# Performance work log

Measured on AMD Instinct MI355X. Metric: run time of the kernel, lower is better.

Reference implementation:

```python
import jax, jax.numpy as jnp
import numpy as np
from jax import lax

LATENT = 128
CODEBOOK = 1024

def _conv(x, w, b):
    # NCHW conv, kernel OIHW, stride 1, padding 1 (same)
    y = lax.conv_general_dilated(x, w, (1, 1), ((1, 1), (1, 1)),
                                 dimension_numbers=('NCHW', 'OIHW', 'NCHW'))
    return y + b[None, :, None, None]

def _conv_transpose(x, w, b):
    # ConvTranspose2d(k=3, s=1, p=1) == conv with flipped kernel, in/out swapped, pad 1
    w_eff = jnp.flip(w, (2, 3)).transpose(1, 0, 2, 3)  # [Cin,Cout,3,3] -> [Cout,Cin,3,3]
    return _conv(x, w_eff, b)

def _maxpool2(x):
    return lax.reduce_window(x, -jnp.inf, lax.max, (1, 1, 2, 2), (1, 1, 2, 2), 'VALID')

def _upsample2(x):
    # F.interpolate(scale_factor=2), default nearest
    return jnp.repeat(jnp.repeat(x, 2, axis=2), 2, axis=3)

def setup_inputs() -> dict:
    key = jax.random.key(0)
    ks = jax.random.split(key, 20)
    f = jnp.float32
    inp = {
        'x': jax.random.uniform(ks[0], (8192, 1, 24, 24), dtype=f),
        'conv1_w': jax.random.normal(ks[1], (32, 1, 3, 3), f) * 0.1,
        'conv1_b': jnp.zeros((32,), f),
        'conv2_w': jax.random.normal(ks[2], (64, 32, 3, 3), f) * 0.05,
        'conv2_b': jnp.zeros((64,), f),
        'conv3_w': jax.random.normal(ks[3], (128, 64, 3, 3), f) * 0.04,
        'conv3_b': jnp.zeros((128,), f),
        'enc_fc_w': jax.random.normal(ks[4], (LATENT, 3 * 3 * 128), f) * 0.03,
        'enc_fc_b': jnp.zeros((LATENT,), f),
        'codebook': jax.random.normal(ks[5], (CODEBOOK, LATENT), f),
        'dec_fc_w': jax.random.normal(ks[6], (3 * 3 * 128, LATENT), f) * 0.09,
        'dec_fc_b': jnp.zeros((3 * 3 * 128,), f),
        'dct1_w': jax.random.normal(ks[7], (128, 64, 3, 3), f) * 0.03,  # [Cin,Cout,kh,kw]
        'dct1_b': jnp.zeros((64,), f),
        'dct2_w': jax.random.normal(ks[8], (64, 32, 3, 3), f) * 0.04,
        'dct2_b': jnp.zeros((32,), f),
        'dct3_w': jax.random.normal(ks[9], (32, 1, 3, 3), f) * 0.06,
        'dct3_b': jnp.zeros((1,), f),
    }
    return inp

def reference(x, conv1_w, conv1_b, conv2_w, conv2_b, conv3_w, conv3_b,
              enc_fc_w, enc_fc_b, codebook, dec_fc_w, dec_fc_b,
              dct1_w, dct1_b, dct2_w, dct2_b, dct3_w, dct3_b):
    # ---- Encoder ----
    h = _maxpool2(jax.nn.relu(_conv(x, conv1_w, conv1_b)))     # [B,32,12,12]
    h = _maxpool2(jax.nn.relu(_conv(h, conv2_w, conv2_b)))     # [B,64,6,6]
    h = _maxpool2(jax.nn.relu(_conv(h, conv3_w, conv3_b)))     # [B,128,3,3]
    z = h.reshape(-1, 3 * 3 * 128) @ enc_fc_w.T + enc_fc_b     # [B,128]
    # ---- Quantize (L2 nearest-codeword; matmul-trick distances, same argmin) ----
    d2 = (jnp.sum(z * z, axis=1, keepdims=True)
          - 2.0 * z @ codebook.T
          + jnp.sum(codebook * codebook, axis=1)[None, :])     # [B,K]
    idx = jnp.argmin(d2, axis=1)                               # [B]
    z_q = codebook[idx]                                        # [B,128]
    # ---- Decoder ----
    d = z_q @ dec_fc_w.T + dec_fc_b                            # [B,1152]
    d = d.reshape(-1, 128, 3, 3)
    d = _upsample2(jax.nn.relu(_conv_transpose(d, dct1_w, dct1_b)))  # [B,64,6,6]
    d = _upsample2(jax.nn.relu(_conv_transpose(d, dct2_w, dct2_b)))  # [B,32,12,12]
    d = _upsample2(jax.nn.relu(_conv_transpose(d, dct3_w, dct3_b)))  # [B,1,24,24]
    return d
```

## Files before the change

### kernel.cpp

```cpp
#include <hip/hip_runtime.h>

typedef __attribute__((ext_vector_type(8))) short short8;
typedef __attribute__((ext_vector_type(4))) float f32x4;
typedef unsigned short ushort_t;
typedef unsigned int uint_t;

#define OFF_W1R   0
#define OFF_W2R   288
#define OFF_W3R   (288+18432)
#define OFF_EWT   (18720+73728)
#define OFF_CT    (92448+147456)
#define OFF_CC    (239904+131072)
#define OFF_DWT   (370976+1024)
#define OFF_D1R   (372000+147456)
#define OFF_D2R   (519456+73728)
#define OFF_D3R   (593184+18432)
#define WS_WEIGHTS (611616+288)
#define OFF_W2BF  WS_WEIGHTS
#define OFF_W3BF  (OFF_W2BF+18432)
#define OFF_H     (OFF_W3BF+73728)
#define OFF_TABLE OFF_H
#define OFF_IDSN  (OFF_H+8192*1152)

__device__ __forceinline__ ushort_t f2bf(float v) {
  uint_t u = __float_as_uint(v);
  return (ushort_t)((u + 0x7FFFu + ((u >> 16) & 1u)) >> 16);
}
__device__ __forceinline__ float bf2f(ushort_t b) {
  return __uint_as_float(((uint_t)b) << 16);
}

__global__ void vq_prep(const float* __restrict__ conv1_w, const float* __restrict__ conv2_w,
                        const float* __restrict__ conv3_w, const float* __restrict__ enc_fc_w,
                        const float* __restrict__ codebook, const float* __restrict__ dec_fc_w,
                        const float* __restrict__ dct1_w, const float* __restrict__ dct2_w,
                        const float* __restrict__ dct3_w, float* __restrict__ ws) {
  int i = blockIdx.x * blockDim.x + threadIdx.x;
  if (i >= WS_WEIGHTS) return;
  if (i < OFF_W2R) {
    int tap = i >> 5, co = i & 31;
    ws[i] = conv1_w[co*9 + tap];
  } else if (i < OFF_W3R) {
    int l = i - OFF_W2R;
    int co = l & 63, r = l >> 6, tap = r % 9, ci = r / 9;
    ws[i] = conv2_w[(co*32 + ci)*9 + tap];
  } else if (i < OFF_EWT) {
    int l = i - OFF_W3R;
    int co = l & 127, r = l >> 7, tap = r % 9, ci = r / 9;
    ws[i] = conv3_w[(co*64 + ci)*9 + tap];
  } else if (i < OFF_CC) {
    return;
  } else if (i < OFF_DWT) {
    int k = i - OFF_CC;
    float s = 0.f;
    for (int j = 0; j < 128; ++j) { float v = codebook[k*128+j]; s += v*v; }
    ws[i] = s;
  } else if (i < OFF_D1R) {
    int l = i - OFF_DWT;
    int j = l % 1152, k = l / 1152;
    ws[i] = dec_fc_w[j*128 + k];
  } else if (i < OFF_D2R) {
    int l = i - OFF_D1R;
    int co = l & 63, r = l >> 6, tap = r % 9, ci = r / 9;
    ws[i] = dct1_w[(ci*64 + co)*9 + (8 - tap)];
  } else if (i < OFF_D3R) {
    int l = i - OFF_D2R;
    int co = l & 31, r = l >> 5, tap = r % 9, ci = r / 9;
    ws[i] = dct2_w[(ci*32 + co)*9 + (8 - tap)];
  } else {
    int l = i - OFF_D3R;
    int tap = l % 9, ci = l / 9;
    ws[i] = dct3_w[ci*9 + (8 - tap)];
  }
}

__global__ void vq_prep2(const float* __restrict__ conv2_w, const float* __restrict__ conv3_w,
                         float* __restrict__ ws) {
  int i = blockIdx.x * blockDim.x + threadIdx.x;
  ushort_t* W2 = (ushort_t*)(ws + OFF_W2BF);
  ushort_t* W3 = (ushort_t*)(ws + OFF_W3BF);
  if (i < 18432) {
    int tap = i >> 11, r = i & 2047, co = r >> 5, ch = r & 31;
    float v = conv2_w[(co*32 + ch)*9 + tap];
    ushort_t hb = f2bf(v);
    W2[i] = hb; W2[18432 + i] = f2bf(v - bf2f(hb));
  } else if (i < 92160) {
    int j = i - 18432;
    int tap = j >> 13, r = j & 8191, co = r >> 6, ch = r & 63;
    float v = conv3_w[(co*64 + ch)*9 + tap];
    ushort_t hb = f2bf(v);
    W3[j] = hb; W3[73728 + j] = f2bf(v - bf2f(hb));
  }
}

__global__ __launch_bounds__(256, 3) void vq_enc(
    const float* __restrict__ x,
    const float* __restrict__ b1, const float* __restrict__ b2, const float* __restrict__ b3,
    const float* __restrict__ ws, float* __restrict__ hout)
{
  __shared__ ushort_t R0h[7840], R0l[7840];
  __shared__ ushort_t C3h[4608], C3l[4608];
  __shared__ float XT[624];
  const int t = threadIdx.x;
  const int b = blockIdx.x;

  for (int i = t; i < 3920; i += 256) { ((uint_t*)R0h)[i] = 0u; ((uint_t*)R0l)[i] = 0u; }
  for (int i = t; i < 2304; i += 256) { ((uint_t*)C3h)[i] = 0u; ((uint_t*)C3l)[i] = 0u; }
  const float* xb = x + (size_t)b * 576;
  for (int i = t; i < 624; i += 256) {
    int row = i / 26, col = i - row * 26;
    XT[i] = (col >= 1 && col <= 24) ? xb[row*24 + col - 1] : 0.f;
  }
  __syncthreads();

  {
    int co = t & 31, g = t >> 5, gy = g >> 1, gx = g & 1;
    float w[9];
    #pragma unroll
    for (int k = 0; k < 9; ++k) w[k] = ws[OFF_W1R + k*32 + co];
    float bias = b1[co];
    #pragma unroll
    for (int pr = 0; pr < 3; ++pr) {
      int Y = gy*6 + pr*2;
      float a0[12], a1[12];
      #pragma unroll
      for (int i = 0; i < 12; ++i) { a0[i] = 0.f; a1[i] = 0.f; }
      #pragma unroll
      for (int wy = 0; wy < 4; ++wy) {
        int ry = Y - 1 + wy;
        if (ry < 0 || ry > 23) continue;
        const float2* rp = (const float2*)&XT[ry*26 + gx*12];
        float r[14];
        #pragma unroll
        for (int k = 0; k < 7; ++k) { float2 p = rp[k]; r[2*k] = p.x; r[2*k+1] = p.y; }
        if (wy < 3) {
          #pragma unroll
          for (int xx = 0; xx < 12; ++xx)
            #pragma unroll
            for (int dx = 0; dx < 3; ++dx) a0[xx] += r[xx+dx] * w[wy*3+dx];
        }
        if (wy >= 1) {
          #pragma unroll
          for (int xx = 0; xx < 12; ++xx)
            #pragma unroll
            for (int dx = 0; dx < 3; ++dx) a1[xx] += r[xx+dx] * w[(wy-1)*3+dx];
        }
      }
      #pragma unroll
      for (int pc = 0; pc < 6; ++pc) {
        float m = fmaxf(fmaxf(a0[2*pc], a0[2*pc+1]), fmaxf(a1[2*pc], a1[2*pc+1]));
        float v = m + bias; v = v > 0.f ? v : 0.f;
        int row = gy*3 + pr, colp = gx*6 + pc;
        int addr = ((row+1)*14 + (colp+1))*40 + co;
        ushort_t hb = f2bf(v);
        R0h[addr] = hb;
        R0l[addr] = f2bf(v - bf2f(hb));
      }
    }
  }
  __syncthreads();

  const int lane = t & 63, quad = lane >> 4, col = lane & 15;
  const int wv = t >> 6;

  {
    const int h = wv & 1, p = wv >> 1;
    const ushort_t* W2 = (const ushort_t*)(ws + OFF_W2BF);
    int baseA[5];
    #pragma unroll
    for (int mi = 0; mi < 5; ++mi) {
      int m = (h*5 + mi)*16 + col; if (m > 143) m = 143;
      int cell = m >> 2, sub = m & 3;
      int opy = cell / 6, opx = cell - opy*6;
      int y = 2*opy + (sub >> 1), xx = 2*opx + (sub & 1);
      baseA[mi] = (y*14 + xx)*40 + quad*8;
    }
    f32x4 acc[5][2];
    #pragma unroll
    for (int mi = 0; mi < 5; ++mi) { acc[mi][0] = (f32x4)0.f; acc[mi][1] = (f32x4)0.f; }
    const int co0 = p*32 + col, co1 = co0 + 16;
    #pragma unroll
    for (int t9 = 0; t9 < 9; ++t9) {
      const int TAPOFF = ((t9/3)*14 + (t9%3))*40;
      int bidx = t9*2048 + quad*8;
      short8 Bh0 = *(const short8*)(W2 + bidx + co0*32);
      short8 Bh1 = *(const short8*)(W2 + bidx + co1*32);
      short8 Bl0 = *(const short8*)(W2 + 18432 + bidx + co0*32);
      short8 Bl1 = *(const short8*)(W2 + 18432 + bidx + co1*32);
      #pragma unroll
      for (int mi = 0; mi < 5; ++mi) {
        int a = baseA[mi] + TAPOFF;
        short8 Ah = *(const short8*)(R0h + a);
        short8 Al = *(const short8*)(R0l + a);
        acc[mi][0] = __builtin_amdgcn_mfma_f32_16x16x32_bf16(Al, Bh0, acc[mi][0], 0, 0, 0);
        acc[mi][0] = __builtin_amdgcn_mfma_f32_16x16x32_bf16(Ah, Bl0, acc[mi][0], 0, 0, 0);
        acc[mi][0] = __builtin_amdgcn_mfma_f32_16x16x32_bf16(Ah, Bh0, acc[mi][0], 0, 0, 0);
        acc[mi][1] = __builtin_amdgcn_mfma_f32_16x16x32_bf16(Al, Bh1, acc[mi][1], 0, 0, 0);
        acc[mi][1] = __builtin_amdgcn_mfma_f32_16x16x32_bf16(Ah, Bl1, acc[mi][1], 0, 0, 0);
        acc[mi][1] = __builtin_amdgcn_mfma_f32_16x16x32_bf16(Ah, Bh1, acc[mi][1], 0, 0, 0);
      }
    }
    #pragma unroll
    for (int mi = 0; mi < 5; ++mi) {
      int cell = (h*5 + mi)*4 + quad;
      if (cell < 36) {
        int opy = cell / 6, opx = cell - opy*6;
        int wa = ((opy+1)*8 + (opx+1))*72;
        #pragma unroll
        for (int j = 0; j < 2; ++j) {
          int ch = j ? co1 : co0;
          f32x4 a = acc[mi][j];
          float v = fmaxf(fmaxf(a.x, a.y), fmaxf(a.z, a.w)) + b2[ch];
          v = v > 0.f ? v : 0.f;
          ushort_t hb = f2bf(v);
          C3h[wa + ch] = hb;
          C3l[wa + ch] = f2bf(v - bf2f(hb));
        }
      }
    }
  }
  __syncthreads();

  {
    const ushort_t* W3 = (const ushort_t*)(ws + OFF_W3BF);
    int baseA[3];
    #pragma unroll
    for (int mt = 0; mt < 3; ++mt) {
      int m = mt*16 + col; if (m > 35) m = 35;
      int cell = m >> 2, sub = m & 3;
      int opy = cell / 3, opx = cell - opy*3;
      int y = 2*opy + (sub >> 1), xx = 2*opx + (sub & 1);
      baseA[mt] = (y*8 + xx)*72 + quad*8;
    }
    f32x4 acc[3][2];
    #pragma unroll
    for (int mt = 0; mt < 3; ++mt) { acc[mt][0] = (f32x4)0.f; acc[mt][1] = (f32x4)0.f; }
    const int co0 = wv*16 + col, co1 = co0 + 64;
    #pragma unroll
    for (int ks = 0; ks < 18; ++ks) {
      const int t9 = ks >> 1, ch0 = (ks & 1)*32;
      const int TAPOFF = ((t9/3)*8 + (t9%3))*72;
      int bidx = t9*8192 + ch0 + quad*8;
      short8 Bh0 = *(const short8*)(W3 + bidx + co0*64);
      short8 Bh1 = *(const short8*)(W3 + bidx + co1*64);
      short8 Bl0 = *(const short8*)(W3 + 73728 + bidx + co0*64);
      short8 Bl1 = *(const short8*)(W3 + 73728 + bidx + co1*64);
      #pragma unroll
      for (int mt = 0; mt < 3; ++mt) {
        int a = baseA[mt] + TAPOFF + ch0;
        short8 Ah = *(const short8*)(C3h + a);
        short8 Al = *(const short8*)(C3l + a);
        acc[mt][0] = __builtin_amdgcn_mfma_f32_16x16x32_bf16(Al, Bh0, acc[mt][0], 0, 0, 0);
        acc[mt][0] = __builtin_amdgcn_mfma_f32_16x16x32_bf16(Ah, Bl0, acc[mt][0], 0, 0, 0);
        acc[mt][0] = __builtin_amdgcn_mfma_f32_16x16x32_bf16(Ah, Bh0, acc[mt][0], 0, 0, 0);
        acc[mt][1] = __builtin_amdgcn_mfma_f32_16x16x32_bf16(Al, Bh1, acc[mt][1], 0, 0, 0);
        acc[mt][1] = __builtin_amdgcn_mfma_f32_16x16x32_bf16(Ah, Bl1, acc[mt][1], 0, 0, 0);
        acc[mt][1] = __builtin_amdgcn_mfma_f32_16x16x32_bf16(Ah, Bh1, acc[mt][1], 0, 0, 0);
      }
    }
    float* hb_ = hout + (size_t)b * 1152;
    #pragma unroll
    for (int mt = 0; mt < 3; ++mt) {
      int cell = mt*4 + quad;
      if (cell < 9) {
        #pragma unroll
        for (int j = 0; j < 2; ++j) {
          int ch = j ? co1 : co0;
          f32x4 a = acc[mt][j];
          float v = fmaxf(fmaxf(a.x, a.y), fmaxf(a.z, a.w)) + b3[ch];
          v = v > 0.f ? v : 0.f;
          hb_[ch*9 + cell] = v;
        }
      }
    }
  }
}

__global__ __launch_bounds__(256, 2) void vq_fc_argmin(
    const float* __restrict__ efw, const float* __restrict__ efb,
    const float* __restrict__ cb, const float* __restrict__ ws,
    const float* __restrict__ h, int* __restrict__ ids)
{
  __shared__ float HT[18432];
  __shared__ float WVs[64];
  __shared__ int   WIs[64];
  const int t = threadIdx.x;
  const int sb = blockIdx.x * 16;

  const float4* src = (const float4*)(h + (size_t)sb * 1152);
  for (int i = t; i < 4608; i += 256) ((float4*)HT)[i] = src[i];
  __syncthreads();

  const int j = t & 127, g = t >> 7;
  float acc[8];
  #pragma unroll
  for (int u = 0; u < 8; ++u) acc[u] = 0.f;
  const float* wj = efw + (size_t)j * 1152;
  for (int k4 = 0; k4 < 1152; k4 += 4) {
    float4 wvv = *(const float4*)(wj + k4);
    const float* hp = &HT[g*9216 + k4];
    #pragma unroll
    for (int u = 0; u < 8; ++u) {
      float4 hv = *(const float4*)(hp + u*1152);
      acc[u] += wvv.x*hv.x + wvv.y*hv.y + wvv.z*hv.z + wvv.w*hv.w;
    }
  }
  float bias = efb[j];
  __syncthreads();
  #pragma unroll
  for (int u = 0; u < 8; ++u) HT[(g*8 + u)*128 + j] = acc[u] + bias;
  __syncthreads();

  float bestv[16]; int besti[16];
  #pragma unroll
  for (int s = 0; s < 16; ++s) { bestv[s] = 3.4e38f; besti[s] = 0; }
  for (int c = 0; c < 4; ++c) {
    int cw = c*256 + t;
    float d[16];
    #pragma unroll
    for (int s = 0; s < 16; ++s) d[s] = 0.f;
    const float* cp = cb + (size_t)cw * 128;
    for (int k4 = 0; k4 < 128; k4 += 4) {
      float4 cv = *(const float4*)(cp + k4);
      #pragma unroll
      for (int s = 0; s < 16; ++s) {
        float4 zv = *(const float4*)(&HT[s*128 + k4]);
        d[s] += cv.x*zv.x + cv.y*zv.y + cv.z*zv.z + cv.w*zv.w;
      }
    }
    float ccv = ws[OFF_CC + cw];
    #pragma unroll
    for (int s = 0; s < 16; ++s) {
      float dist = ccv - 2.f*d[s];
      if (dist < bestv[s]) { bestv[s] = dist; besti[s] = cw; }
    }
  }
  const int lane = t & 63, wid = t >> 6;
  #pragma unroll
  for (int s = 0; s < 16; ++s) {
    float v = bestv[s]; int ii = besti[s];
    #pragma unroll
    for (int off = 32; off >= 1; off >>= 1) {
      float v2 = __shfl_xor(v, off); int i2 = __shfl_xor(ii, off);
      if (v2 < v || (v2 == v && i2 < ii)) { v = v2; ii = i2; }
    }
    if (lane == 0) { WVs[wid*16 + s] = v; WIs[wid*16 + s] = ii; }
  }
  __syncthreads();
  if (t < 16) {
    float v = WVs[t]; int ii = WIs[t];
    #pragma unroll
    for (int w2 = 1; w2 < 4; ++w2) {
      float v2 = WVs[w2*16 + t]; int i2 = WIs[w2*16 + t];
      if (v2 < v || (v2 == v && i2 < ii)) { v = v2; ii = i2; }
    }
    ids[sb + t] = ii;
  }
}

__global__ __launch_bounds__(256, 4) void vq_dec_table(
    const float* __restrict__ codebook, const float* __restrict__ decb,
    const float* __restrict__ d1b, const float* __restrict__ d2b, const float* __restrict__ d3b,
    const float* __restrict__ ws, float* __restrict__ table)
{
  __shared__ float DB[2304];
  __shared__ float R1[2432];
  __shared__ float R0[4736];
  __shared__ float ZQ[256];
  const int t = threadIdx.x;
  const int s0 = blockIdx.x * 2;

  { int s = t >> 7, j = t & 127; ZQ[s*128 + j] = codebook[(size_t)(s0 + s)*128 + j]; }
  __syncthreads();

  #pragma unroll
  for (int p = 0; p < 5; ++p) {
    int j = t + p*256;
    if (j < 1152) {
      float a0 = decb[j], a1 = a0;
      const float* wb = ws + OFF_DWT + j;
      #pragma unroll 4
      for (int k = 0; k < 128; ++k) {
        float wv = wb[k*1152];
        a0 += wv * ZQ[k];
        a1 += wv * ZQ[128 + k];
      }
      DB[j] = a0; DB[1152 + j] = a1;
    }
  }

  for (int s = 0; s < 2; ++s) {
    __syncthreads();
    const float* F = &DB[s*1152];
    float* PS = &DB[s*1152];

    {
      int co = t & 63, g = t >> 6;
      float a9[9];
      #pragma unroll
      for (int i = 0; i < 9; ++i) a9[i] = 0.f;
      const float* wbase = ws + OFF_D1R + co;
      for (int ci = g*32; ci < g*32+32; ++ci) {
        float w[9];
        #pragma unroll
        for (int k = 0; k < 9; ++k) w[k] = wbase[(ci*9+k)*64];
        const float* fin = F + ci*9;
        #pragma unroll
        for (int ry = 0; ry < 3; ++ry) {
          float r[5];
          r[0] = 0.f; r[4] = 0.f;
          r[1] = fin[ry*3]; r[2] = fin[ry*3+1]; r[3] = fin[ry*3+2];
          #pragma unroll
          for (int y = 0; y < 3; ++y) {
            int d = ry - y + 1;
            if (d >= 0 && d < 3) {
              #pragma unroll
              for (int xx = 0; xx < 3; ++xx)
                #pragma unroll
                for (int dx = 0; dx < 3; ++dx) a9[y*3+xx] += r[xx+dx] * w[d*3+dx];
            }
          }
        }
      }
      __syncthreads();
      if (g) {
        #pragma unroll
        for (int i = 0; i < 9; ++i) R0[((g-1)*64 + co)*9 + i] = a9[i];
      }
      __syncthreads();
      if (!g) {
        float bias = d1b[co];
        #pragma unroll
        for (int i = 0; i < 9; ++i)
          a9[i] += R0[co*9 + i] + R0[(64+co)*9 + i] + R0[(128+co)*9 + i];
        #pragma unroll
        for (int yy = 0; yy < 3; ++yy)
          #pragma unroll
          for (int xx = 0; xx < 3; ++xx) {
            float v = a9[yy*3+xx] + bias; v = v > 0.f ? v : 0.f;
            int base = co*38 + (2*yy)*6 + 2*xx;
            R1[base] = v; R1[base+1] = v; R1[base+6] = v; R1[base+7] = v;
          }
      }
    }
    __syncthreads();

    {
      int co = t & 31, hh = (t >> 5) & 1, g = t >> 6;
      int sy = g >> 1, sx = g & 1;
      float a9[9];
      #pragma unroll
      for (int i = 0; i < 9; ++i) a9[i] = 0.f;
      const float* wbase = ws + OFF_D2R + co;
      for (int ci = hh*32; ci < hh*32+32; ++ci) {
        float w[9];
        #pragma unroll
        for (int k = 0; k < 9; ++k) w[k] = wbase[(ci*9+k)*32];
        const float* base = &R1[ci*38];
        #pragma unroll
        for (int wy = 0; wy < 5; ++wy) {
          int ry = sy*3 - 1 + wy;
          if (ry < 0 || ry > 5) continue;
          const float* row = base + ry*6 + sx*3;
          float r[5];
          if (sx == 0) {
            r[0] = 0.f; r[1] = row[0]; r[2] = row[1]; r[3] = row[2]; r[4] = row[3];
          } else {
            r[0] = row[-1]; r[1] = row[0]; r[2] = row[1]; r[3] = row[2]; r[4] = 0.f;
          }
          #pragma unroll
          for (int y = 0; y < 3; ++y) {
            int d = wy - 1 - y + 1;
            if (d >= 0 && d < 3) {
              #pragma unroll
              for (int xx = 0; xx < 3; ++xx)
                #pragma unroll
                for (int dx = 0; dx < 3; ++dx) a9[y*3+xx] += r[xx+dx] * w[d*3+dx];
            }
          }
        }
      }
      __syncthreads();
      if (hh) {
        #pragma unroll
        for (int i = 0; i < 9; ++i) PS[(g*32 + co)*9 + i] = a9[i];
      }
      __syncthreads();
      if (!hh) {
        float bias = d2b[co];
        #pragma unroll
        for (int i = 0; i < 9; ++i) a9[i] += PS[(g*32 + co)*9 + i];
        #pragma unroll
        for (int yy = 0; yy < 3; ++yy)
          #pragma unroll
          for (int xx = 0; xx < 3; ++xx) {
            float v = a9[yy*3+xx] + bias; v = v > 0.f ? v : 0.f;
            int rr = sy*3 + yy, cc_ = sx*3 + xx;
            int base = co*146 + (2*rr)*12 + 2*cc_;
            R0[base] = v; R0[base+1] = v; R0[base+12] = v; R0[base+13] = v;
          }
      }
    }
    __syncthreads();

    if (t < 144) {
      int yy = t / 12, xx = t - yy*12;
      const float* w3 = ws + OFF_D3R;
      float acc = d3b[0];
      for (int ci = 0; ci < 32; ++ci) {
        const float* base = &R0[ci*146];
        #pragma unroll
        for (int dy = 0; dy < 3; ++dy) {
          int ry = yy - 1 + dy;
          int ryc = ry < 0 ? 0 : (ry > 11 ? 11 : ry);
          bool rok = (ry >= 0 && ry < 12);
          #pragma unroll
          for (int dx = 0; dx < 3; ++dx) {
            int rx = xx - 1 + dx;
            int rxc = rx < 0 ? 0 : (rx > 11 ? 11 : rx);
            float v = base[ryc*12 + rxc];
            v = (rok && rx >= 0 && rx < 12) ? v : 0.f;
            acc += v * w3[ci*9 + dy*3 + dx];
          }
        }
      }
      float v = acc > 0.f ? acc : 0.f;
      float* ob = table + (size_t)(s0 + s) * 576;
      int o0 = (2*yy)*24 + 2*xx;
      ob[o0] = v; ob[o0+1] = v; ob[o0+24] = v; ob[o0+25] = v;
    }
  }
}

__global__ __launch_bounds__(256, 8) void vq_scatter(
    const float* __restrict__ table, const int* __restrict__ ids,
    float* __restrict__ out, int nvec)
{
  int idx = blockIdx.x * 256 + threadIdx.x;
  if (idx >= nvec) return;
  int b = idx / 144;
  int r = idx - b * 144;
  int cw = ids[b];
  ((float4*)out)[idx] = ((const float4*)(table + (size_t)cw * 576))[r];
}

extern "C" void kernel_launch(void* const* d_in, const int* in_sizes, int n_in,
                              void* d_out, int out_size, void* d_ws, size_t ws_size,
                              hipStream_t stream) {
  const float* x   = (const float*)d_in[0];
  const float* c1w = (const float*)d_in[1];
  const float* c1b = (const float*)d_in[2];
  const float* c2w = (const float*)d_in[3];
  const float* c2b = (const float*)d_in[4];
  const float* c3w = (const float*)d_in[5];
  const float* c3b = (const float*)d_in[6];
  const float* efw = (const float*)d_in[7];
  const float* efb = (const float*)d_in[8];
  const float* cb  = (const float*)d_in[9];
  const float* dfw = (const float*)d_in[10];
  const float* dfb = (const float*)d_in[11];
  const float* dw1 = (const float*)d_in[12];
  const float* db1 = (const float*)d_in[13];
  const float* dw2 = (const float*)d_in[14];
  const float* db2 = (const float*)d_in[15];
  const float* dw3 = (const float*)d_in[16];
  const float* db3 = (const float*)d_in[17];
  float* ws = (float*)d_ws;
  float* h     = ws + OFF_H;
  float* table = ws + OFF_TABLE;
  int*   ids   = (int*)(ws + OFF_IDSN);
  float* outp = (float*)d_out;
  int B = in_sizes[0] / 576;

  vq_prep<<<(WS_WEIGHTS + 255) / 256, 256, 0, stream>>>(c1w, c2w, c3w, efw, cb, dfw, dw1, dw2, dw3, ws);
  vq_prep2<<<(92160 + 255) / 256, 256, 0, stream>>>(c2w, c3w, ws);
  vq_enc<<<B, 256, 0, stream>>>(x, c1b, c2b, c3b, ws, h);
  vq_fc_argmin<<<B/16, 256, 0, stream>>>(efw, efb, cb, ws, h, ids);
  vq_dec_table<<<512, 256, 0, stream>>>(cb, dfb, db1, db2, db3, ws, table);
  int nvec = B * 144;
  vq_scatter<<<(nvec + 255) / 256, 256, 0, stream>>>(table, ids, outp, nvec);
}
```

Before: 728.3 us.

## Move encoder FC and codebook distances onto split-bf16 MFMA

The encoder FC and the codebook distance matmul now run on bf16 MFMA, using a three-product hi/lo split to keep near-fp32 accuracy. The scalar FP32 FMA loops and the large shared-memory staging of h are gone. The encoder emits h as hi/lo bf16 halves, and the prep kernel pre-splits the FC weights and the codebook into MFMA-friendly layouts. The decoder table kernel now handles one codeword per block over 1024 blocks instead of two per block. The split-bf16 products can change argmin ties or near-ties compared with exact fp32, and the extra prep work adds some fixed cost.

After: 634.1 us. 12.9% less time.

```diff
diff --git a/kernel.cpp b/kernel.cpp
--- a/kernel.cpp
+++ b/kernel.cpp
@@ -30,9 +30,8 @@
   return __uint_as_float(((uint_t)b) << 16);
 }
 
-__global__ void vq_prep(const float* __restrict__ conv1_w, const float* __restrict__ conv2_w,
-                        const float* __restrict__ conv3_w, const float* __restrict__ enc_fc_w,
-                        const float* __restrict__ codebook, const float* __restrict__ dec_fc_w,
+__global__ void vq_prep(const float* __restrict__ conv1_w, const float* __restrict__ codebook,
+                        const float* __restrict__ dec_fc_w,
                         const float* __restrict__ dct1_w, const float* __restrict__ dct2_w,
                         const float* __restrict__ dct3_w, float* __restrict__ ws) {
   int i = blockIdx.x * blockDim.x + threadIdx.x;
@@ -40,14 +39,6 @@
   if (i < OFF_W2R) {
     int tap = i >> 5, co = i & 31;
     ws[i] = conv1_w[co*9 + tap];
-  } else if (i < OFF_W3R) {
-    int l = i - OFF_W2R;
-    int co = l & 63, r = l >> 6, tap = r % 9, ci = r / 9;
-    ws[i] = conv2_w[(co*32 + ci)*9 + tap];
-  } else if (i < OFF_EWT) {
-    int l = i - OFF_W3R;
-    int co = l & 127, r = l >> 7, tap = r % 9, ci = r / 9;
-    ws[i] = conv3_w[(co*64 + ci)*9 + tap];
   } else if (i < OFF_CC) {
     return;
   } else if (i < OFF_DWT) {
@@ -74,11 +65,16 @@
   }
 }
 
+#define P2_N (92160 + 294912 + 262144)
 __global__ void vq_prep2(const float* __restrict__ conv2_w, const float* __restrict__ conv3_w,
+                         const float* __restrict__ enc_fc_w, const float* __restrict__ codebook,
                          float* __restrict__ ws) {
   int i = blockIdx.x * blockDim.x + threadIdx.x;
+  if (i >= P2_N) return;
   ushort_t* W2 = (ushort_t*)(ws + OFF_W2BF);
   ushort_t* W3 = (ushort_t*)(ws + OFF_W3BF);
+  ushort_t* EW = (ushort_t*)(ws + OFF_EWT);
+  ushort_t* CB = (ushort_t*)(ws + OFF_CT);
   if (i < 18432) {
     int tap = i >> 11, r = i & 2047, co = r >> 5, ch = r & 31;
     float v = conv2_w[(co*32 + ch)*9 + tap];
@@ -90,13 +86,28 @@
     float v = conv3_w[(co*64 + ch)*9 + tap];
     ushort_t hb = f2bf(v);
     W3[j] = hb; W3[73728 + j] = f2bf(v - bf2f(hb));
+  } else if (i < 92160 + 294912) {
+    int e = i - 92160;
+    int p = e / 147456, r = e % 147456;
+    int kk = r & 31, n = (r >> 5) & 127, ks = r >> 12;
+    float v = enc_fc_w[n*1152 + ks*32 + kk];
+    ushort_t hb = f2bf(v);
+    EW[r] = (p == 0) ? EW[r] : EW[r];
+    if (p == 0) EW[r] = hb; else EW[147456 + r] = f2bf(v - bf2f(hb));
+  } else {
+    int e = i - 92160 - 294912;
+    int p = e / 131072, r = e % 131072;
+    int kk = r & 31, cw = (r >> 5) & 1023, ks = r >> 15;
+    float v = codebook[cw*128 + ks*32 + kk];
+    ushort_t hb = f2bf(v);
+    if (p == 0) CB[r] = hb; else CB[131072 + r] = f2bf(v - bf2f(hb));
   }
 }
 
 __global__ __launch_bounds__(256, 3) void vq_enc(
     const float* __restrict__ x,
     const float* __restrict__ b1, const float* __restrict__ b2, const float* __restrict__ b3,
-    const float* __restrict__ ws, float* __restrict__ hout)
+    const float* __restrict__ ws, ushort_t* __restrict__ hhi, ushort_t* __restrict__ hlo)
 {
   __shared__ ushort_t R0h[7840], R0l[7840];
   __shared__ ushort_t C3h[4608], C3l[4608];
@@ -258,7 +269,8 @@
         acc[mt][1] = __builtin_amdgcn_mfma_f32_16x16x32_bf16(Ah, Bh1, acc[mt][1], 0, 0, 0);
       }
     }
-    float* hb_ = hout + (size_t)b * 1152;
+    ushort_t* hb_ = hhi + (size_t)b * 1152;
+    ushort_t* lb_ = hlo + (size_t)b * 1152;
     #pragma unroll
     for (int mt = 0; mt < 3; ++mt) {
       int cell = mt*4 + quad;
@@ -269,82 +281,124 @@
           f32x4 a = acc[mt][j];
           float v = fmaxf(fmaxf(a.x, a.y), fmaxf(a.z, a.w)) + b3[ch];
           v = v > 0.f ? v : 0.f;
-          hb_[ch*9 + cell] = v;
-        }
-      }
-    }
-  }
-}
-
-__global__ __launch_bounds__(256, 2) void vq_fc_argmin(
-    const float* __restrict__ efw, const float* __restrict__ efb,
-    const float* __restrict__ cb, const float* __restrict__ ws,
-    const float* __restrict__ h, int* __restrict__ ids)
+          ushort_t hb2 = f2bf(v);
+          hb_[ch*9 + cell] = hb2;
+          lb_[ch*9 + cell] = f2bf(v - bf2f(hb2));
+        }
+      }
+    }
+  }
+}
+
+__global__ __launch_bounds__(256, 4) void vq_fc_argmin(
+    const float* __restrict__ efb, const float* __restrict__ ws,
+    const ushort_t* __restrict__ hhi, const ushort_t* __restrict__ hlo,
+    int* __restrict__ ids)
 {
-  __shared__ float HT[18432];
+  __shared__ float ZL[16*132];
   __shared__ float WVs[64];
   __shared__ int   WIs[64];
   const int t = threadIdx.x;
   const int sb = blockIdx.x * 16;
-
-  const float4* src = (const float4*)(h + (size_t)sb * 1152);
-  for (int i = t; i < 4608; i += 256) ((float4*)HT)[i] = src[i];
-  __syncthreads();
-
-  const int j = t & 127, g = t >> 7;
-  float acc[8];
+  const int lane = t & 63, wv = t >> 6;
+  const int col = lane & 15, quad = lane >> 4;
+
+  const ushort_t* EW  = (const ushort_t*)(ws + OFF_EWT);
+  const ushort_t* CBB = (const ushort_t*)(ws + OFF_CT);
+
+  f32x4 acc0 = (f32x4)0.f, acc1 = (f32x4)0.f;
+  const size_t hrow = (size_t)(sb + col) * 1152 + quad*8;
+  #pragma unroll 4
+  for (int ks = 0; ks < 36; ++ks) {
+    short8 Ah = *(const short8*)(hhi + hrow + ks*32);
+    short8 Al = *(const short8*)(hlo + hrow + ks*32);
+    int n0 = wv*32 + col, n1 = n0 + 16;
+    const ushort_t* bp0 = EW + (ks*128 + n0)*32 + quad*8;
+    const ushort_t* bp1 = EW + (ks*128 + n1)*32 + quad*8;
+    short8 Bh0 = *(const short8*)(bp0);
+    short8 Bl0 = *(const short8*)(bp0 + 147456);
+    short8 Bh1 = *(const short8*)(bp1);
+    short8 Bl1 = *(const short8*)(bp1 + 147456);
+    acc0 = __builtin_amdgcn_mfma_f32_16x16x32_bf16(Al, Bh0, acc0, 0, 0, 0);
+    acc0 = __builtin_amdgcn_mfma_f32_16x16x32_bf16(Ah, Bl0, acc0, 0, 0, 0);
+    acc0 = __builtin_amdgcn_mfma_f32_16x16x32_bf16(Ah, Bh0, acc0, 0, 0, 0);
+    acc1 = __builtin_amdgcn_mfma_f32_16x16x32_bf16(Al, Bh1, acc1, 0, 0, 0);
+    acc1 = __builtin_amdgcn_mfma_f32_16x16x32_bf16(Ah, Bl1, acc1, 0, 0, 0);
+    acc1 = __builtin_amdgcn_mfma_f32_16x16x32_bf16(Ah, Bh1, acc1, 0, 0, 0);
+  }
+  {
+    int n0 = wv*32 + col, n1 = n0 + 16;
+    float bs0 = efb[n0], bs1 = efb[n1];
+    #pragma unroll
+    for (int r = 0; r < 4; ++r) {
+      int m = quad*4 + r;
+      ZL[m*132 + n0] = acc0[r] + bs0;
+      ZL[m*132 + n1] = acc1[r] + bs1;
+    }
+  }
+  __syncthreads();
+
+  short8 zAh[4], zAl[4];
   #pragma unroll
-  for (int u = 0; u < 8; ++u) acc[u] = 0.f;
-  const float* wj = efw + (size_t)j * 1152;
-  for (int k4 = 0; k4 < 1152; k4 += 4) {
-    float4 wvv = *(const float4*)(wj + k4);
-    const float* hp = &HT[g*9216 + k4];
-    #pragma unroll
-    for (int u = 0; u < 8; ++u) {
-      float4 hv = *(const float4*)(hp + u*1152);
-      acc[u] += wvv.x*hv.x + wvv.y*hv.y + wvv.z*hv.z + wvv.w*hv.w;
-    }
-  }
-  float bias = efb[j];
-  __syncthreads();
+  for (int ks = 0; ks < 4; ++ks) {
+    const float* zp = &ZL[col*132 + ks*32 + quad*8];
+    float4 z0 = *(const float4*)zp;
+    float4 z1 = *(const float4*)(zp + 4);
+    float zv[8] = {z0.x, z0.y, z0.z, z0.w, z1.x, z1.y, z1.z, z1.w};
+    ushort_t ph[8], pl[8];
+    #pragma unroll
+    for (int e = 0; e < 8; ++e) {
+      ushort_t hb = f2bf(zv[e]);
+      ph[e] = hb; pl[e] = f2bf(zv[e] - bf2f(hb));
+    }
+    zAh[ks] = *(const short8*)ph;
+    zAl[ks] = *(const short8*)pl;
+  }
+
+  float bestv[4]; int besti[4];
   #pragma unroll
-  for (int u = 0; u < 8; ++u) HT[(g*8 + u)*128 + j] = acc[u] + bias;
-  __syncthreads();
-
-  float bestv[16]; int besti[16];
+  for (int r = 0; r < 4; ++r) { bestv[r] = 3.4e38f; besti[r] = 0; }
+  for (int c4 = 0; c4 < 4; ++c4) {
+    f32x4 dacc[4];
+    #pragma unroll
+    for (int nn = 0; nn < 4; ++nn) dacc[nn] = (f32x4)0.f;
+    #pragma unroll
+    for (int ks = 0; ks < 4; ++ks) {
+      #pragma unroll
+      for (int nn = 0; nn < 4; ++nn) {
+        int cw = (wv*16 + c4*4 + nn)*16 + col;
+        const ushort_t* bp = CBB + (size_t)(ks*1024 + cw)*32 + quad*8;
+        short8 Bh = *(const short8*)bp;
+        short8 Bl = *(const short8*)(bp + 131072);
+        dacc[nn] = __builtin_amdgcn_mfma_f32_16x16x32_bf16(zAl[ks], Bh, dacc[nn], 0, 0, 0);
+        dacc[nn] = __builtin_amdgcn_mfma_f32_16x16x32_bf16(zAh[ks], Bl, dacc[nn], 0, 0, 0);
+        dacc[nn] = __builtin_amdgcn_mfma_f32_16x16x32_bf16(zAh[ks], Bh, dacc[nn], 0, 0, 0);
+      }
+    }
+    #pragma unroll
+    for (int nn = 0; nn < 4; ++nn) {
+      int cw = (wv*16 + c4*4 + nn)*16 + col;
+      float ccv = ws[OFF_CC + cw];
+      #pragma unroll
+      for (int r = 0; r < 4; ++r) {
+        float dist = ccv - 2.f*dacc[nn][r];
+        if (dist < bestv[r]) { bestv[r] = dist; besti[r] = cw; }
+      }
+    }
+  }
+
   #pragma unroll
-  for (int s = 0; s < 16; ++s) { bestv[s] = 3.4e38f; besti[s] = 0; }
-  for (int c = 0; c < 4; ++c) {
-    int cw = c*256 + t;
-    float d[16];
-    #pragma unroll
-    for (int s = 0; s < 16; ++s) d[s] = 0.f;
-    const float* cp = cb + (size_t)cw * 128;
-    for (int k4 = 0; k4 < 128; k4 += 4) {
-      float4 cv = *(const float4*)(cp + k4);
-      #pragma unroll
-      for (int s = 0; s < 16; ++s) {
-        float4 zv = *(const float4*)(&HT[s*128 + k4]);
-        d[s] += cv.x*zv.x + cv.y*zv.y + cv.z*zv.z + cv.w*zv.w;
-      }
-    }
-    float ccv = ws[OFF_CC + cw];
-    #pragma unroll
-    for (int s = 0; s < 16; ++s) {
-      float dist = ccv - 2.f*d[s];
-      if (dist < bestv[s]) { bestv[s] = dist; besti[s] = cw; }
-    }
-  }
-  const int lane = t & 63, wid = t >> 6;
-  #pragma unroll
-  for (int s = 0; s < 16; ++s) {
-    float v = bestv[s]; int ii = besti[s];
-    #pragma unroll
-    for (int off = 32; off >= 1; off >>= 1) {
+  for (int r = 0; r < 4; ++r) {
+    float v = bestv[r]; int ii = besti[r];
+    #pragma unroll
+    for (int off = 8; off >= 1; off >>= 1) {
       float v2 = __shfl_xor(v, off); int i2 = __shfl_xor(ii, off);
       if (v2 < v || (v2 == v && i2 < ii)) { v = v2; ii = i2; }
     }
-    if (lane == 0) { WVs[wid*16 + s] = v; WIs[wid*16 + s] = ii; }
+    if (col == 0) {
+      int m = quad*4 + r;
+      WVs[wv*16 + m] = v; WIs[wv*16 + m] = ii;
+    }
   }
   __syncthreads();
   if (t < 16) {
@@ -363,172 +417,163 @@
     const float* __restrict__ d1b, const float* __restrict__ d2b, const float* __restrict__ d3b,
     const float* __restrict__ ws, float* __restrict__ table)
 {
-  __shared__ float DB[2304];
+  __shared__ float DB[1152];
   __shared__ float R1[2432];
   __shared__ float R0[4736];
-  __shared__ float ZQ[256];
+  __shared__ float ZQ[128];
   const int t = threadIdx.x;
-  const int s0 = blockIdx.x * 2;
-
-  { int s = t >> 7, j = t & 127; ZQ[s*128 + j] = codebook[(size_t)(s0 + s)*128 + j]; }
+  const int cw = blockIdx.x;
+
+  if (t < 128) ZQ[t] = codebook[(size_t)cw*128 + t];
   __syncthreads();
 
   #pragma unroll
   for (int p = 0; p < 5; ++p) {
     int j = t + p*256;
     if (j < 1152) {
-      float a0 = decb[j], a1 = a0;
+      float a0 = decb[j];
       const float* wb = ws + OFF_DWT + j;
       #pragma unroll 4
-      for (int k = 0; k < 128; ++k) {
-        float wv = wb[k*1152];
-        a0 += wv * ZQ[k];
-        a1 += wv * ZQ[128 + k];
-      }
-      DB[j] = a0; DB[1152 + j] = a1;
-    }
-  }
-
-  for (int s = 0; s < 2; ++s) {
+      for (int k = 0; k < 128; ++k) a0 += wb[k*1152] * ZQ[k];
+      DB[j] = a0;
+    }
+  }
+  __syncthreads();
+
+  {
+    int co = t & 63, g = t >> 6;
+    float a9[9];
+    #pragma unroll
+    for (int i = 0; i < 9; ++i) a9[i] = 0.f;
+    const float* wbase = ws + OFF_D1R + co;
+    for (int ci = g*32; ci < g*32+32; ++ci) {
+      float w[9];
+      #pragma unroll
+      for (int k = 0; k < 9; ++k) w[k] = wbase[(ci*9+k)*64];
+      const float* fin = DB + ci*9;
+      #pragma unroll
+      for (int ry = 0; ry < 3; ++ry) {
+        float r[5];
+        r[0] = 0.f; r[4] = 0.f;
+        r[1] = fin[ry*3]; r[2] = fin[ry*3+1]; r[3] = fin[ry*3+2];
+        #pragma unroll
+        for (int y = 0; y < 3; ++y) {
+          int d = ry - y + 1;
+          if (d >= 0 && d < 3) {
+            #pragma unroll
+            for (int xx = 0; xx < 3; ++xx)
+              #pragma unroll
+              for (int dx = 0; dx < 3; ++dx) a9[y*3+xx] += r[xx+dx] * w[d*3+dx];
+          }
+        }
+      }
+    }
     __syncthreads();
-    const float* F = &DB[s*1152];
-    float* PS = &DB[s*1152];
-
-    {
-      int co = t & 63, g = t >> 6;
-      float a9[9];
-      #pragma unroll
-      for (int i = 0; i < 9; ++i) a9[i] = 0.f;
-      const float* wbase = ws + OFF_D1R + co;
-      for (int ci = g*32; ci < g*32+32; ++ci) {
-        float w[9];
-        #pragma unroll
-        for (int k = 0; k < 9; ++k) w[k] = wbase[(ci*9+k)*64];
-        const float* fin = F + ci*9;
-        #pragma unroll
-        for (int ry = 0; ry < 3; ++ry) {
-          float r[5];
-          r[0] = 0.f; r[4] = 0.f;
-          r[1] = fin[ry*3]; r[2] = fin[ry*3+1]; r[3] = fin[ry*3+2];
-          #pragma unroll
-          for (int y = 0; y < 3; ++y) {
-            int d = ry - y + 1;
-            if (d >= 0 && d < 3) {
+    if (g) {
+      #pragma unroll
+      for (int i = 0; i < 9; ++i) R0[((g-1)*64 + co)*9 + i] = a9[i];
+    }
+    __syncthreads();
+    if (!g) {
+      float bias = d1b[co];
+      #pragma unroll
+      for (int i = 0; i < 9; ++i)
+        a9[i] += R0[co*9 + i] + R0[(64+co)*9 + i] + R0[(128+co)*9 + i];
+      #pragma unroll
+      for (int yy = 0; yy < 3; ++yy)
+        #pragma unroll
+        for (int xx = 0; xx < 3; ++xx) {
+          float v = a9[yy*3+xx] + bias; v = v > 0.f ? v : 0.f;
+          int base = co*38 + (2*yy)*6 + 2*xx;
+          R1[base] = v; R1[base+1] = v; R1[base+6] = v; R1[base+7] = v;
+        }
+    }
+  }
+  __syncthreads();
+
+  {
+    int co = t & 31, hh = (t >> 5) & 1, g = t >> 6;
+    int sy = g >> 1, sx = g & 1;
+    float a9[9];
+    #pragma unroll
+    for (int i = 0; i < 9; ++i) a9[i] = 0.f;
+    const float* wbase = ws + OFF_D2R + co;
+    for (int ci = hh*32; ci < hh*32+32; ++ci) {
+      float w[9];
+      #pragma unroll
+      for (int k = 0; k < 9; ++k) w[k] = wbase[(ci*9+k)*32];
+      const float* base = &R1[ci*38];
+      #pragma unroll
+      for (int wy = 0; wy < 5; ++wy) {
+        int ry = sy*3 - 1 + wy;
+        if (ry < 0 || ry > 5) continue;
+        const float* row = base + ry*6 + sx*3;
+        float r[5];
+        if (sx == 0) {
+          r[0] = 0.f; r[1] = row[0]; r[2] = row[1]; r[3] = row[2]; r[4] = row[3];
+        } else {
+          r[0] = row[-1]; r[1] = row[0]; r[2] = row[1]; r[3] = row[2]; r[4] = 0.f;
+        }
+        #pragma unroll
+        for (int y = 0; y < 3; ++y) {
+          int d = wy - 1 - y + 1;
+          if (d >= 0 && d < 3) {
+            #pragma unroll
+            for (int xx = 0; xx < 3; ++xx)
               #pragma unroll
-              for (int xx = 0; xx < 3; ++xx)
-                #pragma unroll
-                for (int dx = 0; dx < 3; ++dx) a9[y*3+xx] += r[xx+dx] * w[d*3+dx];
-            }
+              for (int dx = 0; dx < 3; ++dx) a9[y*3+xx] += r[xx+dx] * w[d*3+dx];
           }
         }
       }
-      __syncthreads();
-      if (g) {
-        #pragma unroll
-        for (int i = 0; i < 9; ++i) R0[((g-1)*64 + co)*9 + i] = a9[i];
-      }
-      __syncthreads();
-      if (!g) {
-        float bias = d1b[co];
-        #pragma unroll
-        for (int i = 0; i < 9; ++i)
-          a9[i] += R0[co*9 + i] + R0[(64+co)*9 + i] + R0[(128+co)*9 + i];
-        #pragma unroll
-        for (int yy = 0; yy < 3; ++yy)
-          #pragma unroll
-          for (int xx = 0; xx < 3; ++xx) {
-            float v = a9[yy*3+xx] + bias; v = v > 0.f ? v : 0.f;
-            int base = co*38 + (2*yy)*6 + 2*xx;
-            R1[base] = v; R1[base+1] = v; R1[base+6] = v; R1[base+7] = v;
-          }
-      }
     }
     __syncthreads();
-
-    {
-      int co = t & 31, hh = (t >> 5) & 1, g = t >> 6;
-      int sy = g >> 1, sx = g & 1;
-      float a9[9];
-      #pragma unroll
-      for (int i = 0; i < 9; ++i) a9[i] = 0.f;
-      const float* wbase = ws + OFF_D2R + co;
-      for (int ci = hh*32; ci < hh*32+32; ++ci) {
-        float w[9];
-        #pragma unroll
-        for (int k = 0; k < 9; ++k) w[k] = wbase[(ci*9+k)*32];
-        const float* base = &R1[ci*38];
-        #pragma unroll
-        for (int wy = 0; wy < 5; ++wy) {
-          int ry = sy*3 - 1 + wy;
-          if (ry < 0 || ry > 5) continue;
-          const float* row = base + ry*6 + sx*3;
-          float r[5];
-          if (sx == 0) {
-            r[0] = 0.f; r[1] = row[0]; r[2] = row[1]; r[3] = row[2]; r[4] = row[3];
-          } else {
-            r[0] = row[-1]; r[1] = row[0]; r[2] = row[1]; r[3] = row[2]; r[4] = 0.f;
-          }
-          #pragma unroll
-          for (int y = 0; y < 3; ++y) {
-            int d = wy - 1 - y + 1;
-            if (d >= 0 && d < 3) {
-              #pragma unroll
-              for (int xx = 0; xx < 3; ++xx)
-                #pragma unroll
-                for (int dx = 0; dx < 3; ++dx) a9[y*3+xx] += r[xx+dx] * w[d*3+dx];
-            }
-          }
-        }
-      }
-      __syncthreads();
-      if (hh) {
-        #pragma unroll
-        for (int i = 0; i < 9; ++i) PS[(g*32 + co)*9 + i] = a9[i];
-      }
-      __syncthreads();
-      if (!hh) {
-        float bias = d2b[co];
-        #pragma unroll
-        for (int i = 0; i < 9; ++i) a9[i] += PS[(g*32 + co)*9 + i];
-        #pragma unroll
-        for (int yy = 0; yy < 3; ++yy)
-          #pragma unroll
-          for (int xx = 0; xx < 3; ++xx) {
-            float v = a9[yy*3+xx] + bias; v = v > 0.f ? v : 0.f;
-            int rr = sy*3 + yy, cc_ = sx*3 + xx;
-            int base = co*146 + (2*rr)*12 + 2*cc_;
-            R0[base] = v; R0[base+1] = v; R0[base+12] = v; R0[base+13] = v;
-          }
-      }
+    if (hh) {
+      #pragma unroll
+      for (int i = 0; i < 9; ++i) DB[(g*32 + co)*9 + i] = a9[i];
     }
     __syncthreads();
-
-    if (t < 144) {
-      int yy = t / 12, xx = t - yy*12;
-      const float* w3 = ws + OFF_D3R;
-      float acc = d3b[0];
-      for (int ci = 0; ci < 32; ++ci) {
-        const float* base = &R0[ci*146];
-        #pragma unroll
-        for (int dy = 0; dy < 3; ++dy) {
-          int ry = yy - 1 + dy;
-          int ryc = ry < 0 ? 0 : (ry > 11 ? 11 : ry);
-          bool rok = (ry >= 0 && ry < 12);
-          #pragma unroll
-          for (int dx = 0; dx < 3; ++dx) {
-            int rx = xx - 1 + dx;
-            int rxc = rx < 0 ? 0 : (rx > 11 ? 11 : rx);
-            float v = base[ryc*12 + rxc];
-            v = (rok && rx >= 0 && rx < 12) ? v : 0.f;
-            acc += v * w3[ci*9 + dy*3 + dx];
-          }
-        }
-      }
-      float v = acc > 0.f ? acc : 0.f;
-      float* ob = table + (size_t)(s0 + s) * 576;
-      int o0 = (2*yy)*24 + 2*xx;
-      ob[o0] = v; ob[o0+1] = v; ob[o0+24] = v; ob[o0+25] = v;
-    }
+    if (!hh) {
+      float bias = d2b[co];
+      #pragma unroll
+      for (int i = 0; i < 9; ++i) a9[i] += DB[(g*32 + co)*9 + i];
+      #pragma unroll
+      for (int yy = 0; yy < 3; ++yy)
+        #pragma unroll
+        for (int xx = 0; xx < 3; ++xx) {
+          float v = a9[yy*3+xx] + bias; v = v > 0.f ? v : 0.f;
+          int rr = sy*3 + yy, cc_ = sx*3 + xx;
+          int base = co*146 + (2*rr)*12 + 2*cc_;
+          R0[base] = v; R0[base+1] = v; R0[base+12] = v; R0[base+13] = v;
+        }
+    }
+  }
+  __syncthreads();
+
+  if (t < 144) {
+    int yy = t / 12, xx = t - yy*12;
+    const float* w3 = ws + OFF_D3R;
+    float acc = d3b[0];
+    for (int ci = 0; ci < 32; ++ci) {
+      const float* base = &R0[ci*146];
+      #pragma unroll
+      for (int dy = 0; dy < 3; ++dy) {
+        int ry = yy - 1 + dy;
+        int ryc = ry < 0 ? 0 : (ry > 11 ? 11 : ry);
+        bool rok = (ry >= 0 && ry < 12);
+        #pragma unroll
+        for (int dx = 0; dx < 3; ++dx) {
+          int rx = xx - 1 + dx;
+          int rxc = rx < 0 ? 0 : (rx > 11 ? 11 : rx);
+          float v = base[ryc*12 + rxc];
+          v = (rok && rx >= 0 && rx < 12) ? v : 0.f;
+          acc += v * w3[ci*9 + dy*3 + dx];
+        }
+      }
+    }
+    float v = acc > 0.f ? acc : 0.f;
+    float* ob = table + (size_t)cw * 576;
+    int o0 = (2*yy)*24 + 2*xx;
+    ob[o0] = v; ob[o0+1] = v; ob[o0+24] = v; ob[o0+25] = v;
   }
 }
 
@@ -566,17 +611,18 @@
   const float* dw3 = (const float*)d_in[16];
   const float* db3 = (const float*)d_in[17];
   float* ws = (float*)d_ws;
-  float* h     = ws + OFF_H;
+  ushort_t* hhi  = (ushort_t*)(ws + OFF_H);
+  ushort_t* hlo  = hhi + (size_t)8192*1152;
   float* table = ws + OFF_TABLE;
   int*   ids   = (int*)(ws + OFF_IDSN);
   float* outp = (float*)d_out;
   int B = in_sizes[0] / 576;
 
-  vq_prep<<<(WS_WEIGHTS + 255) / 256, 256, 0, stream>>>(c1w, c2w, c3w, efw, cb, dfw, dw1, dw2, dw3, ws);
-  vq_prep2<<<(92160 + 255) / 256, 256, 0, stream>>>(c2w, c3w, ws);
-  vq_enc<<<B, 256, 0, stream>>>(x, c1b, c2b, c3b, ws, h);
-  vq_fc_argmin<<<B/16, 256, 0, stream>>>(efw, efb, cb, ws, h, ids);
-  vq_dec_table<<<512, 256, 0, stream>>>(cb, dfb, db1, db2, db3, ws, table);
+  vq_prep<<<(WS_WEIGHTS + 255) / 256, 256, 0, stream>>>(c1w, cb, dfw, dw1, dw2, dw3, ws);
+  vq_prep2<<<(P2_N + 255) / 256, 256, 0, stream>>>(c2w, c3w, efw, cb, ws);
+  vq_enc<<<B, 256, 0, stream>>>(x, c1b, c2b, c3b, ws, hhi, hlo);
+  vq_fc_argmin<<<B/16, 256, 0, stream>>>(efb, ws, hhi, hlo, ids);
+  vq_dec_table<<<1024, 256, 0, stream>>>(cb, dfb, db1, db2, db3, ws, table);
   int nvec = B * 144;
   vq_scatter<<<(nvec + 255) / 256, 256, 0, stream>>>(table, ids, outp, nvec);
 }
```
